# Performance work log

Hardware: AMD Instinct MI355X
Metric: run time of the kernel (lower is better)

## Reference

```python
import jax, jax.numpy as jnp
import numpy as np

NHEADS = 8
HEAD_DIM = 64  # odim // nheads = 512 // 8


def setup_inputs() -> dict:
    key = jax.random.key(0)
    ks = jax.random.split(key, 5)
    B, S, D = 2, 4096, 512
    scale = 1.0 / np.sqrt(D)
    return {
        "m_feats": jax.random.normal(ks[0], (B, S, D), dtype=jnp.float32),
        "Wc": jax.random.normal(ks[1], (2 * D, D), dtype=jnp.float32) * scale,
        "bc": jax.random.normal(ks[2], (2 * D,), dtype=jnp.float32) * 0.01,
        "Wv": jax.random.normal(ks[3], (D, D), dtype=jnp.float32) * scale,
        "bv": jax.random.normal(ks[4], (D,), dtype=jnp.float32) * 0.01,
    }


def reference(m_feats, Wc, bc, Wv, bv):
    # eval mode: dropout(p=0.5) is identity
    B, S, D = m_feats.shape
    H, Dh = NHEADS, HEAD_DIM
    m_k = m_feats @ Wv.T + bv                    # [B,S,D]
    m_trans = m_feats @ Wc.T + bc                # [B,S,2D]
    m_q, m_v = m_trans[..., :D], m_trans[..., D:]
    # torch.split into contiguous per-head chunks == reshape to [B,S,H,Dh]
    k = m_k.reshape(B, S, H, Dh)
    q = m_q.reshape(B, S, H, Dh)
    v = m_v.reshape(B, S, H, Dh)
    # scores[b,h,i,j] = k_i . q_j / sqrt(Dh); softmax over j (the q axis)
    scores = jnp.einsum("bihd,bjhd->bhij", k, q) / np.sqrt(Dh).astype(np.float32)
    w = jax.nn.softmax(scores, axis=-1)          # [B,H,S,S]
    r = jnp.einsum("bhij,bjhd->bihd", w, v).reshape(B, S, D)
    return m_feats + r
```

## Files before the change

### kernel.cpp

```cpp
#include <hip/hip_runtime.h>

#define MTOT 8192

typedef __attribute__((ext_vector_type(8))) short bf16x8;
typedef __attribute__((ext_vector_type(4))) float f32x4;

#if __has_builtin(__builtin_amdgcn_exp2f)
#define EXP2F __builtin_amdgcn_exp2f
#else
#define EXP2F exp2f
#endif

#define SC 0.18033688011112042f
#define LDP 72
#define CTS 136
#define CTQ 72

static __device__ __forceinline__ unsigned short tb(float f) {
  union { float f; unsigned int i; } x;
  x.f = f;
  return (unsigned short)(x.i >> 16);
}
static __device__ __forceinline__ unsigned int pkt(float a, float b) {
  union { float f; unsigned int i; } xa, xb;
  xa.f = a; xb.f = b;
  return (xa.i >> 16) | (xb.i & 0xFFFF0000u);
}
static __device__ __forceinline__ bf16x8 ld8f32_bf16(const float* __restrict__ p) {
  f32x4 lo = *(const f32x4*)p;
  f32x4 hi = *(const f32x4*)(p + 4);
  union { unsigned int u[4]; bf16x8 v; } r;
  r.u[0] = pkt(lo[0], lo[1]);
  r.u[1] = pkt(lo[2], lo[3]);
  r.u[2] = pkt(hi[0], hi[1]);
  r.u[3] = pkt(hi[2], hi[3]);
  return r.v;
}

static __device__ __forceinline__ void stage16(const unsigned short* g,
                                               unsigned short* l, int lane) {
#if __has_builtin(__builtin_amdgcn_global_load_lds)
  __builtin_amdgcn_global_load_lds(
      (const __attribute__((address_space(1))) void*)g,
      (__attribute__((address_space(3))) void*)l, 16, 0, 0);
#else
  *(uint4*)(l + lane * 8) = *(const uint4*)g;
#endif
}

__global__ __launch_bounds__(256) void convert_bf16(
    const float* __restrict__ mf,
    const float* __restrict__ Wc,
    const float* __restrict__ Wv,
    unsigned short* __restrict__ dst)
{
  const size_t NA = (size_t)MTOT * 512;
  const size_t NW = (size_t)1536 * 512;
  const size_t total = (NA + NW) / 8;
  for (size_t u = (size_t)blockIdx.x * blockDim.x + threadIdx.x; u < total;
       u += (size_t)gridDim.x * blockDim.x) {
    const size_t el = u * 8;
    const float* src;
    if (el < NA) {
      src = mf + el;
    } else {
      const size_t e2 = el - NA;
      src = (e2 < (size_t)1024 * 512) ? (Wc + e2) : (Wv + (e2 - (size_t)1024 * 512));
    }
    f32x4 lo = *(const f32x4*)src;
    f32x4 hi = *(const f32x4*)(src + 4);
    uint4 pk;
    pk.x = pkt(lo[0], lo[1]); pk.y = pkt(lo[2], lo[3]);
    pk.z = pkt(hi[0], hi[1]); pk.w = pkt(hi[2], hi[3]);
    *(uint4*)(dst + el) = pk;
  }
}

__global__ __launch_bounds__(256) void gemm_fast(
    const unsigned short* __restrict__ Abf,
    const unsigned short* __restrict__ Wbf,
    const float* __restrict__ bc,
    const float* __restrict__ bv,
    unsigned short* __restrict__ ws)
{
  const int cpx = (int)gridDim.x >> 3;
  const int bid = ((int)blockIdx.x & 7) * cpx + ((int)blockIdx.x >> 3);
  const int tn = bid % 24, tm = bid / 24;
  const int w = threadIdx.x >> 6, lane = threadIdx.x & 63;
  const int n = lane & 15, q = lane >> 4;

  __shared__ alignas(16) unsigned short smem[128 * 64 + 64 * 64];
  unsigned short* As = smem;
  unsigned short* Bs = smem + 128 * 64;

  f32x4 acc[4][2] = {};
  const int rowA0 = tm * 128, colB0 = tn * 64;
  const int lrow = lane >> 3;
  const int sw = ((lane & 7) ^ lrow) * 8;
  const unsigned short* gA = Abf + (size_t)(rowA0 + w * 32 + lrow) * 512 + sw;
  const unsigned short* gB = Wbf + (size_t)(colB0 + w * 16 + lrow) * 512 + sw;

  for (int kc = 0; kc < 512; kc += 64) {
#pragma unroll
    for (int rr = 0; rr < 4; ++rr)
      stage16(gA + (size_t)rr * 8 * 512 + kc, As + (w * 32 + rr * 8) * 64, lane);
#pragma unroll
    for (int rr = 0; rr < 2; ++rr)
      stage16(gB + (size_t)rr * 8 * 512 + kc, Bs + (w * 16 + rr * 8) * 64, lane);
    __syncthreads();
#pragma unroll
    for (int ks = 0; ks < 2; ++ks) {
      const int ch = ((ks * 4 + q) ^ (n & 7)) * 8;
      bf16x8 a[4], b[2];
#pragma unroll
      for (int si = 0; si < 4; ++si)
        a[si] = *(const bf16x8*)(&As[((w >> 1) * 64 + si * 16 + n) * 64 + ch]);
#pragma unroll
      for (int sj = 0; sj < 2; ++sj)
        b[sj] = *(const bf16x8*)(&Bs[((w & 1) * 32 + sj * 16 + n) * 64 + ch]);
#pragma unroll
      for (int si = 0; si < 4; ++si)
#pragma unroll
        for (int sj = 0; sj < 2; ++sj)
          acc[si][sj] = __builtin_amdgcn_mfma_f32_16x16x32_bf16(a[si], b[sj], acc[si][sj], 0, 0, 0);
    }
    __syncthreads();
  }

  unsigned short* Ct = smem;
  const bool isV = (tn >= 8 && tn < 16);
  const int rl0 = (w >> 1) * 64, cl0 = (w & 1) * 32;

  if (!isV) {
    const bool isK = (tn >= 16);
#pragma unroll
    for (int sj = 0; sj < 2; ++sj) {
      const int c = colB0 + cl0 + sj * 16 + n;
      const float bias = isK ? bv[c - 1024] : bc[c];
#pragma unroll
      for (int si = 0; si < 4; ++si)
#pragma unroll
        for (int r = 0; r < 4; ++r) {
          float v = acc[si][sj][r] + bias;
          if (isK) v *= SC;
          Ct[(rl0 + si * 16 + q * 4 + r) * CTQ + cl0 + sj * 16 + n] = tb(v);
        }
    }
  } else {
#pragma unroll
    for (int sj = 0; sj < 2; ++sj) {
      const float bias = bc[colB0 + cl0 + sj * 16 + n];
#pragma unroll
      for (int si = 0; si < 4; ++si) {
        uint2 pk;
        pk.x = pkt(acc[si][sj][0] + bias, acc[si][sj][1] + bias);
        pk.y = pkt(acc[si][sj][2] + bias, acc[si][sj][3] + bias);
        *(uint2*)(&Ct[(cl0 + sj * 16 + n) * CTS + rl0 + si * 16 + q * 4]) = pk;
      }
    }
  }
  __syncthreads();

  if (!isV) {
    const int rk = threadIdx.x & 7, rr2 = threadIdx.x >> 3;
#pragma unroll
    for (int rp = 0; rp < 4; ++rp) {
      const int row = rp * 32 + rr2;
      const int col = rk * 8;
      bf16x8 v = *(const bf16x8*)(&Ct[row * CTQ + col]);
      const int srow = rowA0 + row;
      const int bb = srow >> 12, ss = srow & 4095;
      const int cg = colB0 + col;
      const int cl = (cg >= 1024) ? (cg - 1024) : cg;
      const int hh = cl >> 6, dh0 = cl & 63;
      unsigned short* base = (cg >= 1024) ? (ws + (size_t)2 * MTOT * 512) : ws;
      *(bf16x8*)(base + ((size_t)((bb * 8 + hh) * 4096 + ss)) * 64 + dh0) = v;
    }
  } else {
    const int rk = threadIdx.x & 15, rr2 = threadIdx.x >> 4;
#pragma unroll
    for (int rp = 0; rp < 4; ++rp) {
      const int row = rp * 16 + rr2;
      const int col = rk * 8;
      bf16x8 v = *(const bf16x8*)(&Ct[row * CTS + col]);
      const int cv = (tn - 8) * 64 + row;
      const int hh = cv >> 6, dh0 = cv & 63;
      const int sg = rowA0 + col;
      const int bb = sg >> 12, ss = sg & 4095;
      *(bf16x8*)(ws + (size_t)MTOT * 512 +
                 ((size_t)((bb * 8 + hh) * 64 + dh0)) * 4096 + ss) = v;
    }
  }
}

__global__ __launch_bounds__(256) void gemm_qvk(
    const float* __restrict__ mf,
    const float* __restrict__ Wc,
    const float* __restrict__ bc,
    const float* __restrict__ Wv,
    const float* __restrict__ bv,
    unsigned short* __restrict__ ws,
    int nct)
{
  const int cpx = (int)gridDim.x >> 3;
  const int bid = ((int)blockIdx.x & 7) * cpx + ((int)blockIdx.x >> 3);
  const int tn = bid % nct, tm = bid / nct;
  const int w = threadIdx.x >> 6, lane = threadIdx.x & 63;
  const int n = lane & 15, q = lane >> 4;

  __shared__ alignas(16) unsigned short smem[2 * 128 * LDP];
  unsigned short* As = smem;
  unsigned short* Bs = smem + 128 * LDP;

  f32x4 acc[4][4] = {};
  const int rowA0 = tm * 128, colB0 = tn * 128;
  const int sr = threadIdx.x >> 4;
  const int sc = (threadIdx.x & 15) * 4;

  for (int kc = 0; kc < 512; kc += 64) {
    __syncthreads();
#pragma unroll
    for (int rr = 0; rr < 8; ++rr) {
      const int row = rr * 16 + sr;
      f32x4 av = *(const f32x4*)(mf + (size_t)(rowA0 + row) * 512 + kc + sc);
      uint2 ap; ap.x = pkt(av[0], av[1]); ap.y = pkt(av[2], av[3]);
      *(uint2*)(&As[row * LDP + sc]) = ap;
      const int c = colB0 + row;
      const float* bsrc = (c < 1024) ? (Wc + (size_t)c * 512)
                                     : (Wv + (size_t)(c - 1024) * 512);
      f32x4 bvx = *(const f32x4*)(bsrc + kc + sc);
      uint2 bp; bp.x = pkt(bvx[0], bvx[1]); bp.y = pkt(bvx[2], bvx[3]);
      *(uint2*)(&Bs[row * LDP + sc]) = bp;
    }
    __syncthreads();
#pragma unroll
    for (int ks = 0; ks < 2; ++ks) {
      bf16x8 a[4], b[4];
#pragma unroll
      for (int si = 0; si < 4; ++si)
        a[si] = *(const bf16x8*)(&As[((w >> 1) * 64 + si * 16 + n) * LDP + ks * 32 + q * 8]);
#pragma unroll
      for (int sj = 0; sj < 4; ++sj)
        b[sj] = *(const bf16x8*)(&Bs[((w & 1) * 64 + sj * 16 + n) * LDP + ks * 32 + q * 8]);
#pragma unroll
      for (int si = 0; si < 4; ++si)
#pragma unroll
        for (int sj = 0; sj < 4; ++sj)
          acc[si][sj] = __builtin_amdgcn_mfma_f32_16x16x32_bf16(a[si], b[sj], acc[si][sj], 0, 0, 0);
    }
  }

  __syncthreads();
  unsigned short* Ct = smem;
  const bool isV = (tn >= 4 && tn < 8);
  const int rl0 = (w >> 1) * 64, cl0 = (w & 1) * 64;

  if (!isV) {
    const bool isK = (tn >= 8);
#pragma unroll
    for (int sj = 0; sj < 4; ++sj) {
      const int c = colB0 + sj * 16 + n;
      const float bias = isK ? bv[c - 1024] : bc[c];
#pragma unroll
      for (int si = 0; si < 4; ++si)
#pragma unroll
        for (int r = 0; r < 4; ++r) {
          float v = acc[si][sj][r] + bias;
          if (isK) v *= SC;
          Ct[(rl0 + si * 16 + q * 4 + r) * CTS + cl0 + sj * 16 + n] = tb(v);
        }
    }
  } else {
#pragma unroll
    for (int sj = 0; sj < 4; ++sj) {
      const float bias = bc[colB0 + sj * 16 + n];
#pragma unroll
      for (int si = 0; si < 4; ++si) {
        uint2 pk;
        pk.x = pkt(acc[si][sj][0] + bias, acc[si][sj][1] + bias);
        pk.y = pkt(acc[si][sj][2] + bias, acc[si][sj][3] + bias);
        *(uint2*)(&Ct[(cl0 + sj * 16 + n) * CTS + rl0 + si * 16 + q * 4]) = pk;
      }
    }
  }
  __syncthreads();

  const int rk = threadIdx.x & 7, rr2 = threadIdx.x >> 3;
#pragma unroll
  for (int rp = 0; rp < 4; ++rp) {
    const int row = rp * 32 + rr2;
#pragma unroll
    for (int ch = 0; ch < 2; ++ch) {
      const int col = ch * 64 + rk * 8;
      bf16x8 v = *(const bf16x8*)(&Ct[row * CTS + col]);
      if (!isV) {
        const int srow = rowA0 + row;
        const int bb = srow >> 12, ss = srow & 4095;
        const int cg = colB0 + col;
        const int cl = (cg >= 1024) ? (cg - 1024) : cg;
        const int hh = cl >> 6, dh0 = cl & 63;
        unsigned short* base = (cg >= 1024) ? (ws + (size_t)2 * MTOT * 512) : ws;
        *(bf16x8*)(base + ((size_t)((bb * 8 + hh) * 4096 + ss)) * 64 + dh0) = v;
      } else {
        const int cv = (tn - 4) * 128 + row;
        const int hh = cv >> 6, dh0 = cv & 63;
        const int sg = rowA0 + col;
        const int bb = sg >> 12, ss = sg & 4095;
        *(bf16x8*)(ws + (size_t)MTOT * 512 +
                   ((size_t)((bb * 8 + hh) * 64 + dh0)) * 4096 + ss) = v;
      }
    }
  }
}

template <bool KWS>
__global__ __launch_bounds__(128, 2) void attn_kernel(
    const unsigned short* __restrict__ qvws,
    const float* __restrict__ mf,
    const float* __restrict__ Wv,
    const float* __restrict__ bv,
    float* __restrict__ out)
{
  const int bid = blockIdx.x;
  const int bh = ((bid & 7) << 1) | ((bid >> 3) & 1);
  const int ib = bid >> 4;
  const int b_ = bh >> 3, h = bh & 7;
  const int w = threadIdx.x >> 6, lane = threadIdx.x & 63;
  const int n = lane & 15, q = lane >> 4;
  const int i0 = ib * 64;

  __shared__ alignas(16) unsigned short PK[2][64 * LDP];
  __shared__ float lbuf[2][64];

  const unsigned short* Qb = qvws + (size_t)(bh * 4096) * 64;
  const unsigned short* Vb = qvws + (size_t)MTOT * 512 + (size_t)(bh * 64) * 4096;

  bf16x8 aK[4][2];
  if (KWS) {
    const unsigned short* Kb = qvws + (size_t)2 * MTOT * 512 + (size_t)(bh * 4096) * 64;
#pragma unroll
    for (int sub = 0; sub < 4; ++sub)
#pragma unroll
      for (int s = 0; s < 2; ++s)
        aK[sub][s] = *(const bf16x8*)(Kb + (size_t)(i0 + sub * 16 + n) * 64 + s * 32 + q * 8);
  } else {
    f32x4 ka[2][4] = {};
    for (int kk = 0; kk < 512; kk += 32) {
      bf16x8 a0 = ld8f32_bf16(mf + (size_t)(b_ * 4096 + i0 + (2 * w + 0) * 16 + n) * 512 + kk + q * 8);
      bf16x8 a1 = ld8f32_bf16(mf + (size_t)(b_ * 4096 + i0 + (2 * w + 1) * 16 + n) * 512 + kk + q * 8);
#pragma unroll
      for (int t = 0; t < 4; ++t) {
        bf16x8 bw = ld8f32_bf16(Wv + (size_t)(h * 64 + t * 16 + n) * 512 + kk + q * 8);
        ka[0][t] = __builtin_amdgcn_mfma_f32_16x16x32_bf16(a0, bw, ka[0][t], 0, 0, 0);
        ka[1][t] = __builtin_amdgcn_mfma_f32_16x16x32_bf16(a1, bw, ka[1][t], 0, 0, 0);
      }
    }
#pragma unroll
    for (int sl = 0; sl < 2; ++sl)
#pragma unroll
      for (int t = 0; t < 4; ++t) {
        const float bias = bv[h * 64 + t * 16 + n];
#pragma unroll
        for (int r = 0; r < 4; ++r)
          PK[0][((2 * w + sl) * 16 + q * 4 + r) * LDP + t * 16 + n] =
              tb((ka[sl][t][r] + bias) * SC);
      }
    __syncthreads();
#pragma unroll
    for (int sub = 0; sub < 4; ++sub)
#pragma unroll
      for (int s = 0; s < 2; ++s)
        aK[sub][s] = *(const bf16x8*)(&PK[0][(sub * 16 + n) * LDP + s * 32 + q * 8]);
    __syncthreads();
  }

  f32x4 o[4][4] = {};
  float lsc[4] = {0.0f, 0.0f, 0.0f, 0.0f};
  unsigned short* Pw = &PK[w][0];
  const int jbase = w * 2048;

  bf16x8 bq[4][2], bvv[4][2];
#pragma unroll
  for (int jt = 0; jt < 4; ++jt)
#pragma unroll
    for (int s = 0; s < 2; ++s)
      bq[jt][s] = *(const bf16x8*)(Qb + (size_t)(jbase + jt * 16 + n) * 64 + s * 32 + q * 8);
#pragma unroll
  for (int t = 0; t < 4; ++t)
#pragma unroll
    for (int s = 0; s < 2; ++s)
      bvv[t][s] = *(const bf16x8*)(Vb + (size_t)(t * 16 + n) * 4096 + jbase + s * 32 + q * 8);

  for (int it = 0; it < 32; ++it) {
    const int j1 = jbase + ((it + 1) & 31) * 64;

    f32x4 c[2][4];
#pragma unroll
    for (int jt = 0; jt < 4; ++jt) {
      f32x4 z = {};
      z = __builtin_amdgcn_mfma_f32_16x16x32_bf16(bq[jt][0], aK[0][0], z, 0, 0, 0);
      z = __builtin_amdgcn_mfma_f32_16x16x32_bf16(bq[jt][1], aK[0][1], z, 0, 0, 0);
      c[0][jt] = z;
    }

#pragma unroll
    for (int sub = 0; sub < 4; ++sub) {
      const int cur = sub & 1, nxt = cur ^ 1;
      if (sub < 3) {
#pragma unroll
        for (int jt = 0; jt < 4; ++jt) {
          f32x4 z = {};
          z = __builtin_amdgcn_mfma_f32_16x16x32_bf16(bq[jt][0], aK[sub + 1][0], z, 0, 0, 0);
          z = __builtin_amdgcn_mfma_f32_16x16x32_bf16(bq[jt][1], aK[sub + 1][1], z, 0, 0, 0);
          c[nxt][jt] = z;
        }
      }
      if (sub == 2) {
#pragma unroll
        for (int jt = 0; jt < 4; ++jt)
#pragma unroll
          for (int s = 0; s < 2; ++s)
            bq[jt][s] = *(const bf16x8*)(Qb + (size_t)(j1 + jt * 16 + n) * 64 + s * 32 + q * 8);
      }

#pragma unroll
      for (int jt = 0; jt < 4; ++jt) {
        float e0 = EXP2F(c[cur][jt][0]), e1 = EXP2F(c[cur][jt][1]);
        float e2 = EXP2F(c[cur][jt][2]), e3 = EXP2F(c[cur][jt][3]);
        lsc[sub] += (e0 + e1) + (e2 + e3);
        uint2 pk;
        pk.x = pkt(e0, e1);
        pk.y = pkt(e2, e3);
        *(uint2*)(Pw + (sub * 16 + n) * LDP + jt * 16 + q * 4) = pk;
      }

      asm volatile("s_waitcnt lgkmcnt(0)" ::: "memory");

#pragma unroll
      for (int s = 0; s < 2; ++s) {
        bf16x8 pa = *(const bf16x8*)(Pw + (sub * 16 + n) * LDP + s * 32 + q * 8);
#pragma unroll
        for (int t = 0; t < 4; ++t)
          o[sub][t] = __builtin_amdgcn_mfma_f32_16x16x32_bf16(pa, bvv[t][s], o[sub][t], 0, 0, 0);
      }
    }

#pragma unroll
    for (int t = 0; t < 4; ++t)
#pragma unroll
      for (int s = 0; s < 2; ++s)
        bvv[t][s] = *(const bf16x8*)(Vb + (size_t)(t * 16 + n) * 4096 + j1 + s * 32 + q * 8);
  }

  float lw[4];
#pragma unroll
  for (int sub = 0; sub < 4; ++sub) {
    float v = lsc[sub];
    v += __shfl_xor(v, 16, 64);
    v += __shfl_xor(v, 32, 64);
    lw[sub] = v;
  }

  __syncthreads();
  float* mO = (float*)&PK[0][0];
  const int ebase = (w == 0) ? 0 : 32;
  const int rbase = (w == 0) ? 32 : 0;
  const int esub0 = (w == 0) ? 2 : 0;
  const int ksub0 = (w == 0) ? 0 : 2;
#pragma unroll
  for (int sl = 0; sl < 2; ++sl) {
    const int sub = esub0 + sl;
#pragma unroll
    for (int t = 0; t < 4; ++t)
#pragma unroll
      for (int r = 0; r < 4; ++r)
        mO[(ebase + sl * 16 + q * 4 + r) * 68 + t * 16 + n] = o[sub][t][r];
  }
  if (lane < 16) {
#pragma unroll
    for (int sub = 0; sub < 4; ++sub)
      lbuf[w][sub * 16 + lane] = lw[sub];
  }
  __syncthreads();
#pragma unroll
  for (int sl = 0; sl < 2; ++sl) {
    const int sub = ksub0 + sl;
    float li[4];
#pragma unroll
    for (int r = 0; r < 4; ++r) {
      const int il = sub * 16 + q * 4 + r;
      li[r] = 1.0f / (lbuf[0][il] + lbuf[1][il]);
    }
#pragma unroll
    for (int t = 0; t < 4; ++t) {
#pragma unroll
      for (int r = 0; r < 4; ++r) {
        const int i = i0 + sub * 16 + q * 4 + r;
        const int dh = t * 16 + n;
        const size_t idx = (size_t)(b_ * 4096 + i) * 512 + h * 64 + dh;
        out[idx] = (o[sub][t][r] + mO[(rbase + sl * 16 + q * 4 + r) * 68 + t * 16 + n]) * li[r]
                   + mf[idx];
      }
    }
  }
}

extern "C" void kernel_launch(void* const* d_in, const int* in_sizes, int n_in,
                              void* d_out, int out_size, void* d_ws, size_t ws_size,
                              hipStream_t stream) {
  const float* mf = (const float*)d_in[0];
  const float* Wc = (const float*)d_in[1];
  const float* bc = (const float*)d_in[2];
  const float* Wv = (const float*)d_in[3];
  const float* bv = (const float*)d_in[4];
  float* out = (float*)d_out;
  unsigned short* ws = (unsigned short*)d_ws;

  const size_t elQ = (size_t)MTOT * 512;
  const bool kws = ws_size >= (size_t)3 * elQ * 2;

  if (kws) {
    unsigned short* Abf = (unsigned short*)out;
    unsigned short* Wbf = Abf + (size_t)MTOT * 512;
    convert_bf16<<<2048, 256, 0, stream>>>(mf, Wc, Wv, Abf);
    gemm_fast<<<1536, 256, 0, stream>>>(Abf, Wbf, bc, bv, ws);
    attn_kernel<true><<<1024, 128, 0, stream>>>(ws, mf, Wv, bv, out);
  } else {
    gemm_qvk<<<64 * 8, 256, 0, stream>>>(mf, Wc, bc, Wv, bv, ws, 8);
    attn_kernel<false><<<1024, 128, 0, stream>>>(ws, mf, Wv, bv, out);
  }
}
```

Baseline: 231.2 us.

## Compute K projection inside attention kernel instead of separate GEMM output

```diff
diff --git a/kernel.cpp b/kernel.cpp
--- a/kernel.cpp
+++ b/kernel.cpp
@@ -51,22 +51,15 @@
 __global__ __launch_bounds__(256) void convert_bf16(
     const float* __restrict__ mf,
     const float* __restrict__ Wc,
-    const float* __restrict__ Wv,
     unsigned short* __restrict__ dst)
 {
   const size_t NA = (size_t)MTOT * 512;
-  const size_t NW = (size_t)1536 * 512;
+  const size_t NW = (size_t)1024 * 512;
   const size_t total = (NA + NW) / 8;
   for (size_t u = (size_t)blockIdx.x * blockDim.x + threadIdx.x; u < total;
        u += (size_t)gridDim.x * blockDim.x) {
     const size_t el = u * 8;
-    const float* src;
-    if (el < NA) {
-      src = mf + el;
-    } else {
-      const size_t e2 = el - NA;
-      src = (e2 < (size_t)1024 * 512) ? (Wc + e2) : (Wv + (e2 - (size_t)1024 * 512));
-    }
+    const float* src = (el < NA) ? (mf + el) : (Wc + (el - NA));
     f32x4 lo = *(const f32x4*)src;
     f32x4 hi = *(const f32x4*)(src + 4);
     uint4 pk;
@@ -80,12 +73,11 @@
     const unsigned short* __restrict__ Abf,
     const unsigned short* __restrict__ Wbf,
     const float* __restrict__ bc,
-    const float* __restrict__ bv,
     unsigned short* __restrict__ ws)
 {
   const int cpx = (int)gridDim.x >> 3;
   const int bid = ((int)blockIdx.x & 7) * cpx + ((int)blockIdx.x >> 3);
-  const int tn = bid % 24, tm = bid / 24;
+  const int tn = bid % 16, tm = bid / 16;
   const int w = threadIdx.x >> 6, lane = threadIdx.x & 63;
   const int n = lane & 15, q = lane >> 4;
 
@@ -128,23 +120,19 @@
   }
 
   unsigned short* Ct = smem;
-  const bool isV = (tn >= 8 && tn < 16);
+  const bool isV = (tn >= 8);
   const int rl0 = (w >> 1) * 64, cl0 = (w & 1) * 32;
 
   if (!isV) {
-    const bool isK = (tn >= 16);
 #pragma unroll
     for (int sj = 0; sj < 2; ++sj) {
-      const int c = colB0 + cl0 + sj * 16 + n;
-      const float bias = isK ? bv[c - 1024] : bc[c];
-#pragma unroll
-      for (int si = 0; si < 4; ++si)
-#pragma unroll
-        for (int r = 0; r < 4; ++r) {
-          float v = acc[si][sj][r] + bias;
-          if (isK) v *= SC;
-          Ct[(rl0 + si * 16 + q * 4 + r) * CTQ + cl0 + sj * 16 + n] = tb(v);
-        }
+      const float bias = bc[colB0 + cl0 + sj * 16 + n];
+#pragma unroll
+      for (int si = 0; si < 4; ++si)
+#pragma unroll
+        for (int r = 0; r < 4; ++r)
+          Ct[(rl0 + si * 16 + q * 4 + r) * CTQ + cl0 + sj * 16 + n] =
+              tb(acc[si][sj][r] + bias);
     }
   } else {
 #pragma unroll
@@ -171,10 +159,8 @@
       const int srow = rowA0 + row;
       const int bb = srow >> 12, ss = srow & 4095;
       const int cg = colB0 + col;
-      const int cl = (cg >= 1024) ? (cg - 1024) : cg;
-      const int hh = cl >> 6, dh0 = cl & 63;
-      unsigned short* base = (cg >= 1024) ? (ws + (size_t)2 * MTOT * 512) : ws;
-      *(bf16x8*)(base + ((size_t)((bb * 8 + hh) * 4096 + ss)) * 64 + dh0) = v;
+      const int hh = cg >> 6, dh0 = cg & 63;
+      *(bf16x8*)(ws + ((size_t)((bb * 8 + hh) * 4096 + ss)) * 64 + dh0) = v;
     }
   } else {
     const int rk = threadIdx.x & 15, rr2 = threadIdx.x >> 4;
@@ -197,8 +183,6 @@
     const float* __restrict__ mf,
     const float* __restrict__ Wc,
     const float* __restrict__ bc,
-    const float* __restrict__ Wv,
-    const float* __restrict__ bv,
     unsigned short* __restrict__ ws,
     int nct)
 {
@@ -226,9 +210,7 @@
       uint2 ap; ap.x = pkt(av[0], av[1]); ap.y = pkt(av[2], av[3]);
       *(uint2*)(&As[row * LDP + sc]) = ap;
       const int c = colB0 + row;
-      const float* bsrc = (c < 1024) ? (Wc + (size_t)c * 512)
-                                     : (Wv + (size_t)(c - 1024) * 512);
-      f32x4 bvx = *(const f32x4*)(bsrc + kc + sc);
+      f32x4 bvx = *(const f32x4*)(Wc + (size_t)c * 512 + kc + sc);
       uint2 bp; bp.x = pkt(bvx[0], bvx[1]); bp.y = pkt(bvx[2], bvx[3]);
       *(uint2*)(&Bs[row * LDP + sc]) = bp;
     }
@@ -252,28 +234,24 @@
 
   __syncthreads();
   unsigned short* Ct = smem;
-  const bool isV = (tn >= 4 && tn < 8);
+  const bool isV = (tn >= 4);
   const int rl0 = (w >> 1) * 64, cl0 = (w & 1) * 64;
 
   if (!isV) {
-    const bool isK = (tn >= 8);
 #pragma unroll
     for (int sj = 0; sj < 4; ++sj) {
-      const int c = colB0 + sj * 16 + n;
-      const float bias = isK ? bv[c - 1024] : bc[c];
-#pragma unroll
-      for (int si = 0; si < 4; ++si)
-#pragma unroll
-        for (int r = 0; r < 4; ++r) {
-          float v = acc[si][sj][r] + bias;
-          if (isK) v *= SC;
-          Ct[(rl0 + si * 16 + q * 4 + r) * CTS + cl0 + sj * 16 + n] = tb(v);
-        }
+      const float bias = bc[colB0 + cl0 + sj * 16 + n];
+#pragma unroll
+      for (int si = 0; si < 4; ++si)
+#pragma unroll
+        for (int r = 0; r < 4; ++r)
+          Ct[(rl0 + si * 16 + q * 4 + r) * CTS + cl0 + sj * 16 + n] =
+              tb(acc[si][sj][r] + bias);
     }
   } else {
 #pragma unroll
     for (int sj = 0; sj < 4; ++sj) {
-      const float bias = bc[colB0 + sj * 16 + n];
+      const float bias = bc[colB0 + cl0 + sj * 16 + n];
 #pragma unroll
       for (int si = 0; si < 4; ++si) {
         uint2 pk;
@@ -297,10 +275,8 @@
         const int srow = rowA0 + row;
         const int bb = srow >> 12, ss = srow & 4095;
         const int cg = colB0 + col;
-        const int cl = (cg >= 1024) ? (cg - 1024) : cg;
-        const int hh = cl >> 6, dh0 = cl & 63;
-        unsigned short* base = (cg >= 1024) ? (ws + (size_t)2 * MTOT * 512) : ws;
-        *(bf16x8*)(base + ((size_t)((bb * 8 + hh) * 4096 + ss)) * 64 + dh0) = v;
+        const int hh = cg >> 6, dh0 = cg & 63;
+        *(bf16x8*)(ws + ((size_t)((bb * 8 + hh) * 4096 + ss)) * 64 + dh0) = v;
       } else {
         const int cv = (tn - 4) * 128 + row;
         const int hh = cv >> 6, dh0 = cv & 63;
@@ -313,7 +289,6 @@
   }
 }
 
-template <bool KWS>
 __global__ __launch_bounds__(128, 2) void attn_kernel(
     const unsigned short* __restrict__ qvws,
     const float* __restrict__ mf,
@@ -336,14 +311,7 @@
   const unsigned short* Vb = qvws + (size_t)MTOT * 512 + (size_t)(bh * 64) * 4096;
 
   bf16x8 aK[4][2];
-  if (KWS) {
-    const unsigned short* Kb = qvws + (size_t)2 * MTOT * 512 + (size_t)(bh * 4096) * 64;
-#pragma unroll
-    for (int sub = 0; sub < 4; ++sub)
-#pragma unroll
-      for (int s = 0; s < 2; ++s)
-        aK[sub][s] = *(const bf16x8*)(Kb + (size_t)(i0 + sub * 16 + n) * 64 + s * 32 + q * 8);
-  } else {
+  {
     f32x4 ka[2][4] = {};
     for (int kk = 0; kk < 512; kk += 32) {
       bf16x8 a0 = ld8f32_bf16(mf + (size_t)(b_ * 4096 + i0 + (2 * w + 0) * 16 + n) * 512 + kk + q * 8);
@@ -517,16 +485,15 @@
   unsigned short* ws = (unsigned short*)d_ws;
 
   const size_t elQ = (size_t)MTOT * 512;
-  const bool kws = ws_size >= (size_t)3 * elQ * 2;
-
-  if (kws) {
+  const bool fast = ws_size >= (size_t)2 * elQ * 2;
+
+  if (fast) {
     unsigned short* Abf = (unsigned short*)out;
     unsigned short* Wbf = Abf + (size_t)MTOT * 512;
-    convert_bf16<<<2048, 256, 0, stream>>>(mf, Wc, Wv, Abf);
-    gemm_fast<<<1536, 256, 0, stream>>>(Abf, Wbf, bc, bv, ws);
-    attn_kernel<true><<<1024, 128, 0, stream>>>(ws, mf, Wv, bv, out);
+    convert_bf16<<<2048, 256, 0, stream>>>(mf, Wc, Abf);
+    gemm_fast<<<1024, 256, 0, stream>>>(Abf, Wbf, bc, ws);
   } else {
-    gemm_qvk<<<64 * 8, 256, 0, stream>>>(mf, Wc, bc, Wv, bv, ws, 8);
-    attn_kernel<false><<<1024, 128, 0, stream>>>(ws, mf, Wv, bv, out);
-  }
-}
+    gemm_qvk<<<64 * 8, 256, 0, stream>>>(mf, Wc, bc, ws, 8);
+  }
+  attn_kernel<<<1024, 128, 0, stream>>>(ws, mf, Wv, bv, out);
+}
```

Result: slower. 260.2 us (+12.5%).
